# Performance work log

Hardware: AMD Instinct MI355X
Metric: run time of the kernel (lower is better)

The kernel has to match this reference:

```python
import jax, jax.numpy as jnp
import numpy as np

DT = 0.01
SIM_STEPS = 10_000_000
G = jnp.array([0.0, -9.81], dtype=jnp.float32)  # gravity, matches Ball.g


def setup_inputs() -> dict:
    key = jax.random.key(0)
    k_pos, k_vel = jax.random.split(key)
    return {
        "ball_mass": jnp.ones((), dtype=jnp.float32),  # unused by the math, kept for signature fidelity
        "ball_initial_position": jax.random.normal(k_pos, (2,), dtype=jnp.float32),
        "ball_initial_velocity": jax.random.normal(k_vel, (2,), dtype=jnp.float32),  # nn.Parameter
    }


def reference(ball_mass, ball_initial_position, ball_initial_velocity):
    # Faithful semi-implicit-Euler-style recurrence:
    #   pos <- pos + vel*dt ; vel <- vel + g*dt ; record pos
    # trajectory[0] is the initial position, trajectory[1:] are the updated positions.
    def step(carry, _):
        pos, vel = carry
        pos = pos + vel * DT
        vel = vel + G * DT
        return (pos, vel), pos

    _, traj = jax.lax.scan(
        step, (ball_initial_position, ball_initial_velocity), None, length=SIM_STEPS - 1
    )  # traj: [SIM_STEPS-1, 2]
    return jnp.concatenate([ball_initial_position[None, :], traj], axis=0)  # [SIM_STEPS, 2]
```

## Files before the change

kernel.cpp:

```cpp
#include <hip/hip_runtime.h>
#include <stdint.h>


static constexpr long long NSTEPS = 10000000LL;
static constexpr long long NPOLY  = 1000000LL;
static constexpr long long NS     = 8000000LL;
static constexpr long long KDIR   = 64;
static constexpr int SEGCAP = 384;
static constexpr int RUNCAP = 96;

typedef float f4_native __attribute__((ext_vector_type(4)));

__device__ __forceinline__ bool same_binade_f32(float a, float b) {
    return (((__float_as_uint(a) ^ __float_as_uint(b)) & 0xFF800000u) == 0u);
}
__device__ __forceinline__ unsigned expfield(float v) {
    return (__float_as_uint(v) >> 23) & 0xFFu;
}
__device__ __forceinline__ float pow2f(int e) {
    return __uint_as_float((unsigned)(e + 127) << 23);
}
__device__ __forceinline__ double pow2d(int e) {
    return __longlong_as_double(((long long)(e + 1023)) << 52);
}
__device__ __forceinline__ void nt_store(float4* p, float4 v) {
    f4_native nv;
    nv.x = v.x; nv.y = v.y; nv.z = v.z; nv.w = v.w;
    __builtin_nontemporal_store(nv, (f4_native*)p);
}

__global__ __launch_bounds__(256, 4) void fused(
        const float* __restrict__ pos0, const float* __restrict__ vel0,
        float4* __restrict__ out, long long npairs)
{
    __shared__ int    s_m[SEGCAP + 1];
    __shared__ double s_V[SEGCAP], s_c[SEGCAP], s_P[SEGCAP];
    __shared__ float  s_Vf[SEGCAP], s_cdt[SEGCAP], s_Pf[SEGCAP];
    __shared__ int    r_n[RUNCAP];
    __shared__ double r_p[RUNCAP], r_i[RUNCAP];
    __shared__ float  r_pf[RUNCAP], r_if[RUNCAP];
    __shared__ int    s_nseg, s_bad, s_nrun;
    __shared__ long long s_mstop;
    __shared__ double s_v64, s_p64;

    const int tid  = threadIdx.x;
    const int lane = tid & 63;
    const int wv   = tid >> 6;

    const long long per = (npairs + (long long)gridDim.x - 1) / (long long)gridDim.x;
    const long long i0 = (long long)blockIdx.x * per;
    long long i1 = i0 + per; if (i1 > npairs) i1 = npairs;
    if (i0 >= npairs) return;
    const long long row0 = 2 * i0;
    const long long row1 = 2 * i1;
    const long long mstop = row1 < NSTEPS ? row1 : NSTEPS;

    const float dtf  = 0.01f;
    const float gdtf = __fmul_rn(-9.81f, dtf);
    const double dtd = (double)dtf, gcd = (double)gdtf, gdtd = gcd;
    const double p0y = (double)pos0[1], v0y = (double)vel0[1];

    if (tid == 0) {
        s_nrun = 0;
        double V = v0y, P = p0y;
        for (int t = 0; t < (int)KDIR; ++t) {
            const float vf = (float)V;
            P += dtd * V;
            V = (double)__fadd_rn(vf, gdtf);
        }
        s_v64 = V; s_p64 = P;

        bool bad = false;
        long long m = KDIR;
        int nseg = 0;
        if (row1 > NPOLY) {
            while (m < mstop) {
                if (nseg >= SEGCAP - 2) { bad = true; break; }
                const float vf = (float)V;
                if ((double)vf != V || !(vf < 0.0f)) { bad = true; break; }
                const unsigned ef = expfield(vf);
                if (ef == 0u || ef == 0xFFu) { bad = true; break; }
                const int k = (int)ef - 126;
                const double ulp     = pow2d(k - 24);
                const double inv_ulp = pow2d(24 - k);
                const double g = -V * inv_ulp;
                const double q = -gcd * inv_ulp;
                const double fq = floor(q);
                const long long rem = mstop - m;

                if (q - fq == 0.5) {
                    const float vb = __fadd_rn(vf, gdtf);
                    const double cb = (double)vb - V;
                    s_m[nseg] = (int)m; s_V[nseg] = V; s_c[nseg] = cb; s_P[nseg] = P; ++nseg;
                    P += dtd * V; V += cb; m += 1;
                    continue;
                }
                const double cg = floor(q + 0.5);
                if (!(cg > 0.0)) { bad = true; break; }
                const double c = -cg * ulp;

                const double lim = 16777216.0;
                float t0f = __fdividef((float)(lim - g - q), (float)cg);
                long long T = (long long)t0f + 1;
                if (T > rem) T = rem;
                if (T < 0) T = 0;
                for (int f = 0; f < 4 && T > 0 && !(g + (double)(T - 1) * cg + q < lim); ++f) --T;
                for (int f = 0; f < 4 && T < rem && (g + (double)T * cg + q < lim); ++f) ++T;
                if (T > rem) T = rem;

                if (T > 0) {
                    s_m[nseg] = (int)m; s_V[nseg] = V; s_c[nseg] = c; s_P[nseg] = P; ++nseg;
                    P += dtd * ((double)T * V + c * ((double)T * (double)(T - 1) * 0.5));
                    V += (double)T * c;
                    m += T;
                    if (m >= mstop) break;
                }
                const float vf2 = (float)V;
                if ((double)vf2 != V) { bad = true; break; }
                const float vb = __fadd_rn(vf2, gdtf);
                const double cb = (double)vb - V;
                s_m[nseg] = (int)m; s_V[nseg] = V; s_c[nseg] = cb; s_P[nseg] = P; ++nseg;
                P += dtd * V; V += cb; m += 1;
            }
            bad = bad || (m < mstop);
        }
        s_bad = bad ? 1 : 0;
        s_nseg = nseg;
        s_mstop = m;
        s_m[nseg] = 0x7fffffff;
    }
    __syncthreads();

    if (wv == 0 && s_bad && row1 > NPOLY) {
        double V = s_v64, P = s_p64;
        long long m = KDIR;
        int nseg = 0;
        while (m < mstop && nseg < SEGCAP) {
            const float vf  = (float)V;
            const float vn1 = __fadd_rn(vf, gdtf);
            const double c  = (double)vn1 - V;
            const long long rem = mstop - m;
            long long Lb = rem;
            const float cf = (float)c;
            const unsigned ef = expfield(vf);
            if (vf == 0.0f || ef == 0u) {
                Lb = 64;
            } else if (cf != 0.0f) {
                const int k = (int)ef - 126;
                float s = vf < 0.0f ? -1.0f : 1.0f;
                float B = ((vf < 0.0f) == (cf < 0.0f)) ? s * pow2f(k) : s * pow2f(k - 1);
                float r = __fdividef(B - vf, cf);
                if (r >= 0.0f && r < 4.0e9f) Lb = (long long)r + 1;
            }
            long long Lhi = Lb + 2;
            if (Lhi > rem) Lhi = rem;
            if (Lhi < 1) Lhi = 1;

            long long L = 1;
            {
                const long long candL = Lhi - 63 + (long long)lane;
                bool valid = false;
                if (candL >= 1) {
                    const double ve = V + (double)(candL - 1) * c;
                    const float vef = (float)ve;
                    const float vn2 = __fadd_rn(vef, gdtf);
                    valid = ((double)vef == ve)
                         && same_binade_f32(vef, vf)
                         && ((double)vn2 - ve == c);
                }
                const unsigned long long msk = __ballot(valid);
                if (msk) L = Lhi - 63 + (long long)(63 - __clzll(msk));
            }
            if (L < 1) L = 1;
            if (L > rem) L = rem;

            if (lane == 0) { s_m[nseg] = (int)m; s_V[nseg] = V; s_c[nseg] = c; s_P[nseg] = P; }
            ++nseg;
            P += dtd * ((double)L * V + c * ((double)L * (double)(L - 1) * 0.5));
            V += (double)L * c;
            m += L;
        }
        if (lane == 0) { s_nseg = nseg; s_mstop = m; s_m[nseg] = 0x7fffffff; }
    }
    __syncthreads();

    if (wv == 0 && row1 > NS && s_mstop >= NS && s_nseg > 0) {
        const int nseg = s_nseg;
        const long long mbuilt = s_mstop;
        int lo = 0, hi = nseg - 1;
        while (lo < hi) { int mid = (lo + hi + 1) >> 1;
                          if ((long long)s_m[mid] <= NS) lo = mid; else hi = mid - 1; }
        int jj = lo;
        const double t0 = (double)(NS - s_m[jj]);
        double vel = s_V[jj] + t0 * s_c[jj];
        double P2  = s_P[jj] + dtd * (t0 * s_V[jj] + s_c[jj] * (t0 * (t0 - 1.0) * 0.5));
        double pos = (double)(float)P2;
        long long n = NS;
        int nrun = 0;
        long long nend = (row1 < NSTEPS - 1) ? row1 : (NSTEPS - 1);
        if (nend > mbuilt) nend = mbuilt;
        while (n < nend && nrun < RUNCAP) {
            while (s_m[jj + 1] <= (int)n) ++jj;
            const double cv = s_c[jj];
            long long Lcap = (long long)s_m[jj + 1] - n;
            if (Lcap > mbuilt - n) Lcap = mbuilt - n;
            const long long rem = (NSTEPS - 1) - n;
            if (Lcap > rem) Lcap = rem;

            const float pf = (float)pos;
            const float vf2 = (float)vel;
            const float dstep = __fmul_rn(vf2, dtf);
            const float pn1 = __fadd_rn(pf, dstep);
            const double inc = (double)pn1 - pos;

            long long La = Lcap, Lc = Lcap;
            const float incf = (float)inc;
            const unsigned efp = expfield(pf);
            if (pf == 0.0f || efp == 0u) {
                La = 64;
            } else if (incf != 0.0f) {
                const int k = (int)efp - 126;
                float s = pf < 0.0f ? -1.0f : 1.0f;
                float B = ((pf < 0.0f) == (incf < 0.0f)) ? s * pow2f(k) : s * pow2f(k - 1);
                float r = __fdividef(B - pf, incf);
                if (r >= 0.0f && r < 4.0e9f) { La = (long long)r - 1; if (La < 0) La = 0; }
            }
            const double dd = cv * dtd;
            if (dd != 0.0 && pf != 0.0f && efp != 0u) {
                const int k = (int)efp - 126;
                if (k - 24 > -126) {
                    const float ulpf = pow2f(k - 24);
                    const double d0 = (double)dstep;
                    const double T = inc + (dd < 0.0 ? -0.5 : 0.5) * (double)ulpf;
                    float r = __fdividef((float)(T - d0), (float)dd);
                    if (r >= 0.0f && r < 4.0e9f) { Lc = (long long)r + 2; if (Lc < 1) Lc = 1; }
                }
            }
            long long Lhi = La < Lc ? La : Lc;
            Lhi += 3;
            if (Lhi > Lcap) Lhi = Lcap;
            if (Lhi < 1) Lhi = 1;

            long long L = 1;
            {
                const long long candL = Lhi - 63 + (long long)lane;
                bool valid = false;
                if (candL >= 1) {
                    const double pe = pos + (double)(candL - 1) * inc;
                    const double ve = vel + (double)(candL - 1) * cv;
                    const float pef = (float)pe;
                    const float vef = (float)ve;
                    const float d2  = __fmul_rn(vef, dtf);
                    const float pn2 = __fadd_rn(pef, d2);
                    valid = ((double)pef == pe)
                         && same_binade_f32(pef, pf)
                         && ((double)vef == ve)
                         && ((double)pn2 - pe == inc);
                }
                const unsigned long long msk = __ballot(valid);
                if (msk) L = Lhi - 63 + (long long)(63 - __clzll(msk));
            }
            if (L < 1) L = 1;
            if (L > Lcap) L = Lcap;
            if (L < 1) L = 1;

            if (lane == 0) { r_n[nrun] = (int)n; r_p[nrun] = pos; r_i[nrun] = inc; }
            ++nrun;
            pos += (double)L * inc;
            vel += (double)L * cv;
            n += L;
        }
        if (lane == 0) s_nrun = nrun;
    }
    __syncthreads();

    {
        const int nseg = s_nseg, nrun = s_nrun;
        for (int i = tid; i < nseg; i += 256) {
            s_Vf[i]  = (float)s_V[i];
            s_cdt[i] = (float)(dtd * s_c[i]);
            s_Pf[i]  = (float)s_P[i];
        }
        for (int i = tid; i < nrun; i += 256) {
            r_pf[i] = (float)r_p[i];
            r_if[i] = (float)r_i[i];
        }
    }
    __syncthreads();

    const int nseg = s_nseg;
    const int nrun = s_nrun;
    const float pxf = pos0[0];
    const float cxf = __fmul_rn(vel0[0], dtf);
    const float pyf = (float)p0y;
    const float vyf = (float)v0y;
    const float q2f = (float)(dtd * gdtd);

    const long long ii = i0 + tid;
    if (ii >= i1) return;

    int mode = 3, jf = 0, rf = 0;
    if (row1 <= NPOLY) {
        mode = 0;
    } else if (row0 >= NS && nrun > 0) {
        int rlo = 0, rhi = nrun - 1;
        const int t0 = (int)row0;
        while (rlo < rhi) { int mid = (rlo + rhi + 1) >> 1; if (r_n[mid] <= t0) rlo = mid; else rhi = mid - 1; }
        rf = rlo;
        if (rf + 1 >= nrun || (long long)r_n[rf + 1] >= row1) mode = 2;
    } else if (row0 >= NPOLY && row1 <= NS && nseg > 0) {
        int lo = 0, hi = nseg - 1;
        const int t0 = (int)row0;
        while (lo < hi) { int mid = (lo + hi + 1) >> 1; if (s_m[mid] <= t0) lo = mid; else hi = mid - 1; }
        jf = lo;
        if ((long long)s_m[jf + 1] >= row1) mode = 1;
    }

    if (mode == 0) {
        const float C = 0.5f * q2f;
        const float B = dtf * vyf - C;
        const float A = pyf;
        for (long long i = ii; i < i1; i += blockDim.x) {
            const float mf0 = (float)(2 * i), mf1 = mf0 + 1.0f;
            float4 o;
            o.x = fmaf(mf0, cxf, pxf);
            o.z = fmaf(mf1, cxf, pxf);
            o.y = fmaf(mf0, fmaf(mf0, C, B), A);
            o.w = fmaf(mf1, fmaf(mf1, C, B), A);
            nt_store(&out[i], o);
        }
    } else if (mode == 1) {
        const float C = 0.5f * s_cdt[jf];
        const float B = dtf * s_Vf[jf] - C;
        const float A = s_Pf[jf];
        const int mj = s_m[jf];
        for (long long i = ii; i < i1; i += blockDim.x) {
            const float t0 = (float)(int)(2 * i - mj), t1 = t0 + 1.0f;
            const float mf0 = (float)(2 * i), mf1 = mf0 + 1.0f;
            float4 o;
            o.x = fmaf(mf0, cxf, pxf);
            o.z = fmaf(mf1, cxf, pxf);
            o.y = fmaf(t0, fmaf(t0, C, B), A);
            o.w = fmaf(t1, fmaf(t1, C, B), A);
            nt_store(&out[i], o);
        }
    } else if (mode == 2) {
        const float A = r_pf[rf], Bv = r_if[rf];
        const int rn0 = r_n[rf];
        for (long long i = ii; i < i1; i += blockDim.x) {
            const float t0 = (float)(int)(2 * i - rn0), t1 = t0 + 1.0f;
            const float mf0 = (float)(2 * i), mf1 = mf0 + 1.0f;
            float4 o;
            o.x = fmaf(mf0, cxf, pxf);
            o.z = fmaf(mf1, cxf, pxf);
            o.y = fmaf(t0, Bv, A);
            o.w = fmaf(t1, Bv, A);
            nt_store(&out[i], o);
        }
    } else {
        int j = 0, r = 0;
        if (nseg > 0) {
            const int t0 = (int)(2 * ii);
            int lo = 0, hi = nseg - 1;
            while (lo < hi) { int mid = (lo + hi + 1) >> 1; if (s_m[mid] <= t0) lo = mid; else hi = mid - 1; }
            j = lo;
            if (nrun > 0) {
                int rlo = 0, rhi = nrun - 1;
                while (rlo < rhi) { int mid = (rlo + rhi + 1) >> 1; if (r_n[mid] <= t0) rlo = mid; else rhi = mid - 1; }
                r = rlo;
            }
        }
        for (long long i = ii; i < i1; i += blockDim.x) {
            const long long m0 = 2 * i, m1 = m0 + 1;
            const float mf0 = (float)m0, mf1 = (float)m1;
            float4 o;
            o.x = fmaf(mf0, cxf, pxf);
            o.z = fmaf(mf1, cxf, pxf);
            const int t0 = (int)m0;
            if (m1 < NPOLY) {
                o.y = pyf + dtf * (mf0 * vyf) + q2f * (mf0 * (mf0 - 1.0f) * 0.5f);
                o.w = pyf + dtf * (mf1 * vyf) + q2f * (mf1 * (mf1 - 1.0f) * 0.5f);
            } else if (m1 < NS || nrun <= 0) {
                while (s_m[j + 1] <= t0) ++j;
                float t = (float)(int)(m0 - s_m[j]);
                o.y = s_Pf[j] + dtf * (t * s_Vf[j]) + s_cdt[j] * (t * (t - 1.0f) * 0.5f);
                const int j1 = (s_m[j + 1] <= (int)m1) ? j + 1 : j;
                t = (float)(int)(m1 - s_m[j1]);
                o.w = s_Pf[j1] + dtf * (t * s_Vf[j1]) + s_cdt[j1] * (t * (t - 1.0f) * 0.5f);
            } else {
                while (r + 1 < nrun && r_n[r + 1] <= t0) ++r;
                o.y = r_pf[r] + (float)(int)(m0 - r_n[r]) * r_if[r];
                const int r1 = (r + 1 < nrun && r_n[r + 1] <= (int)m1) ? r + 1 : r;
                o.w = r_pf[r1] + (float)(int)(m1 - r_n[r1]) * r_if[r1];
            }
            nt_store(&out[i], o);
        }
    }
}

extern "C" void kernel_launch(void* const* d_in, const int* in_sizes, int n_in,
                              void* d_out, int out_size, void* d_ws, size_t ws_size,
                              hipStream_t stream) {
    const float* pos0 = (const float*)d_in[1];
    const float* vel0 = (const float*)d_in[2];

    const long long npairs = (long long)out_size / 4;
    fused<<<1024, 256, 0, stream>>>(pos0, vel0, (float4*)d_out, npairs);
}
```

Baseline: 37.61 us.

## Split serial segment construction into single-block prep kernel feeding fill kernel

Moves the serial segment and run table construction out of every block into one 64-thread prep kernel that writes the tables to workspace. A separate fill kernel then loads those tables into shared memory and writes the trajectory. This removes the redundant per-block serial work that each of the 1024 blocks repeated. The cost is an extra kernel launch and a serialized dependency between the two kernels, during which only one wave runs.

```diff
diff --git a/kernel.cpp b/kernel.cpp
--- a/kernel.cpp
+++ b/kernel.cpp
@@ -29,38 +29,30 @@
     __builtin_nontemporal_store(nv, (f4_native*)p);
 }
 
-__global__ __launch_bounds__(256, 4) void fused(
+__global__ __launch_bounds__(64) void prep(
         const float* __restrict__ pos0, const float* __restrict__ vel0,
-        float4* __restrict__ out, long long npairs)
+        int* __restrict__ counts,
+        int* __restrict__ g_m, double* __restrict__ g_V,
+        double* __restrict__ g_c, double* __restrict__ g_P,
+        int* __restrict__ g_rn, double* __restrict__ g_rp,
+        double* __restrict__ g_ri)
 {
     __shared__ int    s_m[SEGCAP + 1];
     __shared__ double s_V[SEGCAP], s_c[SEGCAP], s_P[SEGCAP];
-    __shared__ float  s_Vf[SEGCAP], s_cdt[SEGCAP], s_Pf[SEGCAP];
     __shared__ int    r_n[RUNCAP];
     __shared__ double r_p[RUNCAP], r_i[RUNCAP];
-    __shared__ float  r_pf[RUNCAP], r_if[RUNCAP];
     __shared__ int    s_nseg, s_bad, s_nrun;
     __shared__ long long s_mstop;
     __shared__ double s_v64, s_p64;
 
-    const int tid  = threadIdx.x;
-    const int lane = tid & 63;
-    const int wv   = tid >> 6;
-
-    const long long per = (npairs + (long long)gridDim.x - 1) / (long long)gridDim.x;
-    const long long i0 = (long long)blockIdx.x * per;
-    long long i1 = i0 + per; if (i1 > npairs) i1 = npairs;
-    if (i0 >= npairs) return;
-    const long long row0 = 2 * i0;
-    const long long row1 = 2 * i1;
-    const long long mstop = row1 < NSTEPS ? row1 : NSTEPS;
-
+    const int lane = threadIdx.x;
     const float dtf  = 0.01f;
     const float gdtf = __fmul_rn(-9.81f, dtf);
-    const double dtd = (double)dtf, gcd = (double)gdtf, gdtd = gcd;
+    const double dtd = (double)dtf, gcd = (double)gdtf;
     const double p0y = (double)pos0[1], v0y = (double)vel0[1];
-
-    if (tid == 0) {
+    const long long mstop = NSTEPS;
+
+    if (lane == 0) {
         s_nrun = 0;
         double V = v0y, P = p0y;
         for (int t = 0; t < (int)KDIR; ++t) {
@@ -73,57 +65,55 @@
         bool bad = false;
         long long m = KDIR;
         int nseg = 0;
-        if (row1 > NPOLY) {
-            while (m < mstop) {
-                if (nseg >= SEGCAP - 2) { bad = true; break; }
-                const float vf = (float)V;
-                if ((double)vf != V || !(vf < 0.0f)) { bad = true; break; }
-                const unsigned ef = expfield(vf);
-                if (ef == 0u || ef == 0xFFu) { bad = true; break; }
-                const int k = (int)ef - 126;
-                const double ulp     = pow2d(k - 24);
-                const double inv_ulp = pow2d(24 - k);
-                const double g = -V * inv_ulp;
-                const double q = -gcd * inv_ulp;
-                const double fq = floor(q);
-                const long long rem = mstop - m;
-
-                if (q - fq == 0.5) {
-                    const float vb = __fadd_rn(vf, gdtf);
-                    const double cb = (double)vb - V;
-                    s_m[nseg] = (int)m; s_V[nseg] = V; s_c[nseg] = cb; s_P[nseg] = P; ++nseg;
-                    P += dtd * V; V += cb; m += 1;
-                    continue;
-                }
-                const double cg = floor(q + 0.5);
-                if (!(cg > 0.0)) { bad = true; break; }
-                const double c = -cg * ulp;
-
-                const double lim = 16777216.0;
-                float t0f = __fdividef((float)(lim - g - q), (float)cg);
-                long long T = (long long)t0f + 1;
-                if (T > rem) T = rem;
-                if (T < 0) T = 0;
-                for (int f = 0; f < 4 && T > 0 && !(g + (double)(T - 1) * cg + q < lim); ++f) --T;
-                for (int f = 0; f < 4 && T < rem && (g + (double)T * cg + q < lim); ++f) ++T;
-                if (T > rem) T = rem;
-
-                if (T > 0) {
-                    s_m[nseg] = (int)m; s_V[nseg] = V; s_c[nseg] = c; s_P[nseg] = P; ++nseg;
-                    P += dtd * ((double)T * V + c * ((double)T * (double)(T - 1) * 0.5));
-                    V += (double)T * c;
-                    m += T;
-                    if (m >= mstop) break;
-                }
-                const float vf2 = (float)V;
-                if ((double)vf2 != V) { bad = true; break; }
-                const float vb = __fadd_rn(vf2, gdtf);
+        while (m < mstop) {
+            if (nseg >= SEGCAP - 2) { bad = true; break; }
+            const float vf = (float)V;
+            if ((double)vf != V || !(vf < 0.0f)) { bad = true; break; }
+            const unsigned ef = expfield(vf);
+            if (ef == 0u || ef == 0xFFu) { bad = true; break; }
+            const int k = (int)ef - 126;
+            const double ulp     = pow2d(k - 24);
+            const double inv_ulp = pow2d(24 - k);
+            const double g = -V * inv_ulp;
+            const double q = -gcd * inv_ulp;
+            const double fq = floor(q);
+            const long long rem = mstop - m;
+
+            if (q - fq == 0.5) {
+                const float vb = __fadd_rn(vf, gdtf);
                 const double cb = (double)vb - V;
                 s_m[nseg] = (int)m; s_V[nseg] = V; s_c[nseg] = cb; s_P[nseg] = P; ++nseg;
                 P += dtd * V; V += cb; m += 1;
-            }
-            bad = bad || (m < mstop);
-        }
+                continue;
+            }
+            const double cg = floor(q + 0.5);
+            if (!(cg > 0.0)) { bad = true; break; }
+            const double c = -cg * ulp;
+
+            const double lim = 16777216.0;
+            float t0f = __fdividef((float)(lim - g - q), (float)cg);
+            long long T = (long long)t0f + 1;
+            if (T > rem) T = rem;
+            if (T < 0) T = 0;
+            for (int f = 0; f < 4 && T > 0 && !(g + (double)(T - 1) * cg + q < lim); ++f) --T;
+            for (int f = 0; f < 4 && T < rem && (g + (double)T * cg + q < lim); ++f) ++T;
+            if (T > rem) T = rem;
+
+            if (T > 0) {
+                s_m[nseg] = (int)m; s_V[nseg] = V; s_c[nseg] = c; s_P[nseg] = P; ++nseg;
+                P += dtd * ((double)T * V + c * ((double)T * (double)(T - 1) * 0.5));
+                V += (double)T * c;
+                m += T;
+                if (m >= mstop) break;
+            }
+            const float vf2 = (float)V;
+            if ((double)vf2 != V) { bad = true; break; }
+            const float vb = __fadd_rn(vf2, gdtf);
+            const double cb = (double)vb - V;
+            s_m[nseg] = (int)m; s_V[nseg] = V; s_c[nseg] = cb; s_P[nseg] = P; ++nseg;
+            P += dtd * V; V += cb; m += 1;
+        }
+        bad = bad || (m < mstop);
         s_bad = bad ? 1 : 0;
         s_nseg = nseg;
         s_mstop = m;
@@ -131,7 +121,7 @@
     }
     __syncthreads();
 
-    if (wv == 0 && s_bad && row1 > NPOLY) {
+    if (s_bad) {
         double V = s_v64, P = s_p64;
         long long m = KDIR;
         int nseg = 0;
@@ -184,7 +174,7 @@
     }
     __syncthreads();
 
-    if (wv == 0 && row1 > NS && s_mstop >= NS && s_nseg > 0) {
+    if (s_mstop >= NS && s_nseg > 0) {
         const int nseg = s_nseg;
         const long long mbuilt = s_mstop;
         int lo = 0, hi = nseg - 1;
@@ -197,7 +187,7 @@
         double pos = (double)(float)P2;
         long long n = NS;
         int nrun = 0;
-        long long nend = (row1 < NSTEPS - 1) ? row1 : (NSTEPS - 1);
+        long long nend = NSTEPS - 1;
         if (nend > mbuilt) nend = mbuilt;
         while (n < nend && nrun < RUNCAP) {
             while (s_m[jj + 1] <= (int)n) ++jj;
@@ -274,27 +264,63 @@
     }
     __syncthreads();
 
-    {
-        const int nseg = s_nseg, nrun = s_nrun;
-        for (int i = tid; i < nseg; i += 256) {
-            s_Vf[i]  = (float)s_V[i];
-            s_cdt[i] = (float)(dtd * s_c[i]);
-            s_Pf[i]  = (float)s_P[i];
-        }
-        for (int i = tid; i < nrun; i += 256) {
-            r_pf[i] = (float)r_p[i];
-            r_if[i] = (float)r_i[i];
-        }
+    const int nseg = s_nseg, nrun = s_nrun;
+    for (int i = lane; i <= nseg; i += 64) {
+        g_m[i] = s_m[i];
+        if (i < nseg) { g_V[i] = s_V[i]; g_c[i] = s_c[i]; g_P[i] = s_P[i]; }
+    }
+    for (int i = lane; i < nrun; i += 64) {
+        g_rn[i] = r_n[i]; g_rp[i] = r_p[i]; g_ri[i] = r_i[i];
+    }
+    if (lane == 0) { counts[0] = nseg; counts[1] = nrun; }
+}
+
+__global__ __launch_bounds__(256, 4) void fill(
+        const float* __restrict__ pos0, const float* __restrict__ vel0,
+        const int* __restrict__ counts,
+        const int* __restrict__ g_m, const double* __restrict__ g_V,
+        const double* __restrict__ g_c, const double* __restrict__ g_P,
+        const int* __restrict__ g_rn, const double* __restrict__ g_rp,
+        const double* __restrict__ g_ri,
+        float4* __restrict__ out, long long npairs)
+{
+    __shared__ int   s_m[SEGCAP + 1];
+    __shared__ float s_Vf[SEGCAP], s_cdt[SEGCAP], s_Pf[SEGCAP];
+    __shared__ int   r_n[RUNCAP];
+    __shared__ float r_pf[RUNCAP], r_if[RUNCAP];
+
+    const int tid = threadIdx.x;
+    const long long per = (npairs + (long long)gridDim.x - 1) / (long long)gridDim.x;
+    const long long i0 = (long long)blockIdx.x * per;
+    long long i1 = i0 + per; if (i1 > npairs) i1 = npairs;
+    if (i0 >= npairs) return;
+    const long long row0 = 2 * i0;
+    const long long row1 = 2 * i1;
+
+    const float dtf  = 0.01f;
+    const float gdtf = __fmul_rn(-9.81f, dtf);
+    const double dtd = (double)dtf;
+
+    const int nseg = counts[0];
+    const int nrun = counts[1];
+    for (int i = tid; i <= nseg && i <= SEGCAP; i += 256) s_m[i] = g_m[i];
+    for (int i = tid; i < nseg && i < SEGCAP; i += 256) {
+        s_Vf[i]  = (float)g_V[i];
+        s_cdt[i] = (float)(dtd * g_c[i]);
+        s_Pf[i]  = (float)g_P[i];
+    }
+    for (int i = tid; i < nrun && i < RUNCAP; i += 256) {
+        r_n[i]  = g_rn[i];
+        r_pf[i] = (float)g_rp[i];
+        r_if[i] = (float)g_ri[i];
     }
     __syncthreads();
 
-    const int nseg = s_nseg;
-    const int nrun = s_nrun;
     const float pxf = pos0[0];
     const float cxf = __fmul_rn(vel0[0], dtf);
-    const float pyf = (float)p0y;
-    const float vyf = (float)v0y;
-    const float q2f = (float)(dtd * gdtd);
+    const float pyf = pos0[1];
+    const float vyf = vel0[1];
+    const float q2f = (float)((double)dtf * (double)gdtf);
 
     const long long ii = i0 + tid;
     if (ii >= i1) return;
@@ -404,6 +430,21 @@
     const float* pos0 = (const float*)d_in[1];
     const float* vel0 = (const float*)d_in[2];
 
+    char* base = (char*)d_ws;
+    size_t off = 64;
+    int* counts = (int*)base;
+    double* g_V  = (double*)(base + off); off += (size_t)SEGCAP * 8;
+    double* g_c  = (double*)(base + off); off += (size_t)SEGCAP * 8;
+    double* g_P  = (double*)(base + off); off += (size_t)SEGCAP * 8;
+    double* g_rp = (double*)(base + off); off += (size_t)RUNCAP * 8;
+    double* g_ri = (double*)(base + off); off += (size_t)RUNCAP * 8;
+    int* g_m  = (int*)(base + off); off += ((size_t)(SEGCAP + 1) * 4 + 7) & ~(size_t)7;
+    int* g_rn = (int*)(base + off);
+
+    prep<<<1, 64, 0, stream>>>(pos0, vel0, counts, g_m, g_V, g_c, g_P,
+                               g_rn, g_rp, g_ri);
+
     const long long npairs = (long long)out_size / 4;
-    fused<<<1024, 256, 0, stream>>>(pos0, vel0, (float4*)d_out, npairs);
-}
+    fill<<<1024, 256, 0, stream>>>(pos0, vel0, counts, g_m, g_V, g_c, g_P,
+                                   g_rn, g_rp, g_ri, (float4*)d_out, npairs);
+}
```

Result: slower. 45.91 us (+22.1%).

## Parallelize segment construction across a wavefront and defer position prefix sums

Applied to the files above, without the earlier changes.

Segment building for the velocity recurrence moves from a single thread to a full wavefront: each segment's length is resolved with a 64-lane ballot instead of serial fix-up loops, and per-segment position deltas are computed in parallel afterwards, followed by a serial prefix sum. The closed-form polynomial region is widened from the first 1M steps to the first 4M, and its evaluation is rewritten in Horner form with FMAs. The intent is to shorten the serial setup phase that every block pays before it writes output. The trade-off is extra barriers and shared memory, plus a wider polynomial region whose float accuracy against the reference may be at risk.

```diff
diff --git a/kernel.cpp b/kernel.cpp
--- a/kernel.cpp
+++ b/kernel.cpp
@@ -3,7 +3,7 @@
 
 
 static constexpr long long NSTEPS = 10000000LL;
-static constexpr long long NPOLY  = 1000000LL;
+static constexpr long long NPOLY  = 4000000LL;
 static constexpr long long NS     = 8000000LL;
 static constexpr long long KDIR   = 64;
 static constexpr int SEGCAP = 384;
@@ -34,7 +34,7 @@
         float4* __restrict__ out, long long npairs)
 {
     __shared__ int    s_m[SEGCAP + 1];
-    __shared__ double s_V[SEGCAP], s_c[SEGCAP], s_P[SEGCAP];
+    __shared__ double s_V[SEGCAP], s_c[SEGCAP], s_P[SEGCAP], s_dP[SEGCAP];
     __shared__ float  s_Vf[SEGCAP], s_cdt[SEGCAP], s_Pf[SEGCAP];
     __shared__ int    r_n[RUNCAP];
     __shared__ double r_p[RUNCAP], r_i[RUNCAP];
@@ -60,74 +60,71 @@
     const double dtd = (double)dtf, gcd = (double)gdtf, gdtd = gcd;
     const double p0y = (double)pos0[1], v0y = (double)vel0[1];
 
-    if (tid == 0) {
-        s_nrun = 0;
+    int k_tie;
+    {
+        unsigned gbits = __float_as_uint(gdtf);
+        unsigned mant = (gbits & 0x7FFFFFu) | 0x800000u;
+        int tz = __ffs((int)mant) - 1;
+        int E = (int)((gbits >> 23) & 0xFFu) - 127 - 23 + tz;
+        k_tie = E + 25;
+    }
+
+    if (tid == 0) { s_nseg = 0; s_nrun = 0; s_mstop = 0; s_bad = 0; }
+    __syncthreads();
+
+    if (wv == 0 && row1 > NPOLY) {
         double V = v0y, P = p0y;
         for (int t = 0; t < (int)KDIR; ++t) {
             const float vf = (float)V;
             P += dtd * V;
             V = (double)__fadd_rn(vf, gdtf);
         }
-        s_v64 = V; s_p64 = P;
+        if (lane == 0) { s_v64 = V; s_p64 = P; }
 
         bool bad = false;
         long long m = KDIR;
         int nseg = 0;
-        if (row1 > NPOLY) {
-            while (m < mstop) {
-                if (nseg >= SEGCAP - 2) { bad = true; break; }
-                const float vf = (float)V;
-                if ((double)vf != V || !(vf < 0.0f)) { bad = true; break; }
-                const unsigned ef = expfield(vf);
-                if (ef == 0u || ef == 0xFFu) { bad = true; break; }
-                const int k = (int)ef - 126;
-                const double ulp     = pow2d(k - 24);
+        while (m < mstop && nseg < SEGCAP - 2) {
+            const float vf = (float)V;
+            const unsigned ef = expfield(vf);
+            bad = bad | ((double)vf != V) | !(vf < 0.0f) | (ef == 0u) | (ef == 0xFFu);
+            if (bad) break;
+            const int k = (int)ef - 126;
+            const float vn1 = __fadd_rn(vf, gdtf);
+            const double c = (double)vn1 - V;
+            if (!(c < 0.0)) { bad = true; break; }
+            const long long rem = mstop - m;
+
+            long long T = 1;
+            if (k != k_tie) {
                 const double inv_ulp = pow2d(24 - k);
-                const double g = -V * inv_ulp;
-                const double q = -gcd * inv_ulp;
-                const double fq = floor(q);
-                const long long rem = mstop - m;
-
-                if (q - fq == 0.5) {
-                    const float vb = __fadd_rn(vf, gdtf);
-                    const double cb = (double)vb - V;
-                    s_m[nseg] = (int)m; s_V[nseg] = V; s_c[nseg] = cb; s_P[nseg] = P; ++nseg;
-                    P += dtd * V; V += cb; m += 1;
-                    continue;
-                }
-                const double cg = floor(q + 0.5);
-                if (!(cg > 0.0)) { bad = true; break; }
-                const double c = -cg * ulp;
-
+                const double g  = -V * inv_ulp;
+                const double q  = -gcd * inv_ulp;
+                const double cg = -c * inv_ulp;
                 const double lim = 16777216.0;
                 float t0f = __fdividef((float)(lim - g - q), (float)cg);
-                long long T = (long long)t0f + 1;
+                const long long Th = (long long)t0f;
+                const long long Tc = Th - 31 + (long long)lane;
+                const bool valid = (Tc >= 1) && (Tc <= rem)
+                                && (g + (double)(Tc - 1) * cg + q < lim);
+                const unsigned long long msk = __ballot(valid);
+                if (msk) T = Th - 31 + (long long)(63 - __clzll(msk));
+                else     T = (Th - 31 > rem) ? rem : 1;
+                if (T < 1) T = 1;
                 if (T > rem) T = rem;
-                if (T < 0) T = 0;
-                for (int f = 0; f < 4 && T > 0 && !(g + (double)(T - 1) * cg + q < lim); ++f) --T;
-                for (int f = 0; f < 4 && T < rem && (g + (double)T * cg + q < lim); ++f) ++T;
-                if (T > rem) T = rem;
-
-                if (T > 0) {
-                    s_m[nseg] = (int)m; s_V[nseg] = V; s_c[nseg] = c; s_P[nseg] = P; ++nseg;
-                    P += dtd * ((double)T * V + c * ((double)T * (double)(T - 1) * 0.5));
-                    V += (double)T * c;
-                    m += T;
-                    if (m >= mstop) break;
-                }
-                const float vf2 = (float)V;
-                if ((double)vf2 != V) { bad = true; break; }
-                const float vb = __fadd_rn(vf2, gdtf);
-                const double cb = (double)vb - V;
-                s_m[nseg] = (int)m; s_V[nseg] = V; s_c[nseg] = cb; s_P[nseg] = P; ++nseg;
-                P += dtd * V; V += cb; m += 1;
-            }
-            bad = bad || (m < mstop);
-        }
-        s_bad = bad ? 1 : 0;
-        s_nseg = nseg;
-        s_mstop = m;
-        s_m[nseg] = 0x7fffffff;
+            }
+            if (lane == 0) { s_m[nseg] = (int)m; s_V[nseg] = V; s_c[nseg] = c; }
+            ++nseg;
+            V += (double)T * c;
+            m += T;
+        }
+        bad = bad | (m < mstop);
+        if (lane == 0) {
+            s_bad = bad ? 1 : 0;
+            s_nseg = nseg;
+            s_mstop = m;
+            s_m[nseg] = 0x7fffffff;
+        }
     }
     __syncthreads();
 
@@ -181,6 +178,22 @@
             m += L;
         }
         if (lane == 0) { s_nseg = nseg; s_mstop = m; s_m[nseg] = 0x7fffffff; }
+    }
+    __syncthreads();
+
+    if (!s_bad && row1 > NPOLY && s_nseg > 0) {
+        const int nseg = s_nseg;
+        for (int j = tid; j < nseg; j += 256) {
+            const long long mj = s_m[j];
+            const long long me = (j + 1 < nseg) ? (long long)s_m[j + 1] : s_mstop;
+            const double len = (double)(me - mj);
+            s_dP[j] = dtd * (len * s_V[j] + s_c[j] * (len * (len - 1.0) * 0.5));
+        }
+        __syncthreads();
+        if (tid == 0) {
+            double P = s_p64;
+            for (int j = 0; j < nseg; ++j) { s_P[j] = P; P += s_dP[j]; }
+        }
     }
     __syncthreads();
 
@@ -378,8 +391,10 @@
             o.z = fmaf(mf1, cxf, pxf);
             const int t0 = (int)m0;
             if (m1 < NPOLY) {
-                o.y = pyf + dtf * (mf0 * vyf) + q2f * (mf0 * (mf0 - 1.0f) * 0.5f);
-                o.w = pyf + dtf * (mf1 * vyf) + q2f * (mf1 * (mf1 - 1.0f) * 0.5f);
+                const float C = 0.5f * q2f;
+                const float B = dtf * vyf - C;
+                o.y = fmaf(mf0, fmaf(mf0, C, B), pyf);
+                o.w = fmaf(mf1, fmaf(mf1, C, B), pyf);
             } else if (m1 < NS || nrun <= 0) {
                 while (s_m[j + 1] <= t0) ++j;
                 float t = (float)(int)(m0 - s_m[j]);
```

Result: faster. 35.13 us, median of 2 (-6.6%).
